# Kernel optimization log

Measured on AMD Instinct MI355X. Metric: run time of the kernel, lower is better.

Reference implementation:

```python
import jax, jax.numpy as jnp
import numpy as np

B, S, HID = 2, 2048, 2048
H, HKV, D = 8, 4, 256
SW = 1024
SOFTCAP = 50.0
SCALE = D ** -0.5
NEG = -2.3819763e38
ROPE_BASE = 10000.0


def _rope(x, cos, sin):
    # x: [B, S, H, D]; cos/sin: [S, D/2]. Gemma: first half real, second half imag.
    d2 = x.shape[-1] // 2
    x1, x2 = x[..., :d2], x[..., d2:]
    c = cos[None, :, None, :]
    s = sin[None, :, None, :]
    return jnp.concatenate([x1 * c - x2 * s, x1 * s + x2 * c], axis=-1)


def setup_inputs() -> dict:
    key = jax.random.key(0)
    k1, k2, k3, k4, k5, k6 = jax.random.split(key, 6)
    hidden_states = jax.random.normal(k1, (B, S, HID), dtype=jnp.float32)
    # Gemma RoPE freqs_cis -> cos/sin tables [S, D/2]
    inv_freq = 1.0 / (ROPE_BASE ** (np.arange(0, D, 2, dtype=np.float32) / D))
    t = np.arange(S, dtype=np.float32)
    ang = np.outer(t, inv_freq)  # [S, D/2]
    freqs_cos = jnp.asarray(np.cos(ang), dtype=jnp.float32)
    freqs_sin = jnp.asarray(np.sin(ang), dtype=jnp.float32)
    # causal additive mask [1,1,S,S]
    i = jnp.arange(S)
    causal = i[:, None] >= i[None, :]
    mask = jnp.where(causal, 0.0, NEG).astype(jnp.float32)[None, None]
    std = HID ** -0.5
    wq = jax.random.normal(k2, (H * D, HID), dtype=jnp.float32) * std
    wk = jax.random.normal(k3, (HKV * D, HID), dtype=jnp.float32) * std
    wv = jax.random.normal(k4, (HKV * D, HID), dtype=jnp.float32) * std
    wo = jax.random.normal(k5, (HID, H * D), dtype=jnp.float32) * (H * D) ** -0.5
    return {"hidden_states": hidden_states, "freqs_cos": freqs_cos,
            "freqs_sin": freqs_sin, "mask": mask,
            "wq": wq, "wk": wk, "wv": wv, "wo": wo}


def reference(hidden_states, freqs_cos, freqs_sin, mask, wq, wk, wv, wo):
    b, s, _ = hidden_states.shape
    q = (hidden_states @ wq.T).reshape(b, s, H, D)
    k = (hidden_states @ wk.T).reshape(b, s, HKV, D)
    v = (hidden_states @ wv.T).reshape(b, s, HKV, D)
    q = _rope(q, freqs_cos, freqs_sin)
    k = _rope(k, freqs_cos, freqs_sin)
    # GQA: repeat_interleave kv heads to match query heads
    rep = H // HKV
    k = jnp.repeat(k, rep, axis=2)
    v = jnp.repeat(v, rep, axis=2)
    q = q.transpose(0, 2, 1, 3)  # [B,H,S,D]
    k = k.transpose(0, 2, 1, 3)
    v = v.transpose(0, 2, 1, 3)
    # local (sliding window) mask: keep |i-j| <= SW-1, else NEG
    i = jnp.arange(s)
    rel = i[:, None] - i[None, :]
    sliding = jnp.abs(rel) < SW
    mask = jnp.where(sliding[None, None], mask, NEG)
    # scaled scores with tanh logit softcapping
    scores = jnp.einsum('bhqd,bhkd->bhqk', q * SCALE, k)
    scores = jnp.tanh(scores / SOFTCAP) * SOFTCAP
    scores = scores + mask
    probs = jax.nn.softmax(scores.astype(jnp.float32), axis=-1).astype(q.dtype)
    attn_output = jnp.einsum('bhqk,bhkd->bhqd', probs, v)  # [B,H,S,D]
    out = attn_output.transpose(0, 2, 1, 3).reshape(b, s, H * D) @ wo.T
    return out, probs, attn_output
```

## Files before the change

### kernel.cpp

```cpp
#include <hip/hip_runtime.h>
#include <hip/hip_bf16.h>

typedef __bf16 bfx8 __attribute__((ext_vector_type(8)));
typedef float  floatx4 __attribute__((ext_vector_type(4)));

#define B_   2
#define S_   2048
#define HID_ 2048
#define H_   8
#define HKV_ 4
#define D_   256
#define SW_  1024
#define NTOK (B_*S_)

__device__ __forceinline__ bool inputs_are_f32(const void* fc) {
  return *(const unsigned int*)fc == 0x3F800000u;
}

__device__ __forceinline__ bfx8 cvt8(const float* p) {
  floatx4 a = *(const floatx4*)p, b = *(const floatx4*)(p + 4);
  bfx8 r;
#pragma unroll
  for (int i = 0; i < 4; ++i) { r[i] = (__bf16)a[i]; r[i + 4] = (__bf16)b[i]; }
  return r;
}

__device__ __forceinline__ bfx8 ld8(const void* base, size_t eoff, bool f32m) {
  if (f32m) return cvt8((const float*)base + eoff);
  return *(const bfx8*)((const __bf16*)base + eoff);
}

__global__ __launch_bounds__(256)
void cvt_f32_bf16(const void* __restrict__ in, __bf16* __restrict__ out,
                  int n8, const void* __restrict__ fcp)
{
  const bool f32m = inputs_are_f32(fcp);
  int i = blockIdx.x * 256 + threadIdx.x;
  int stride = gridDim.x * 256;
  for (; i < n8; i += stride) {
    if (f32m) ((bfx8*)out)[i] = cvt8((const float*)in + (size_t)i * 8);
    else      ((bfx8*)out)[i] = ((const bfx8*)in)[i];
  }
}

template<int SWZ>
__device__ __forceinline__ void xcd_tile(int& bx, int& by) {
  int gx = gridDim.x;
  int orig = blockIdx.y * gx + blockIdx.x;
  int xcd = orig & 7, loc = orig >> 3;
  if (SWZ == 1) {
    int wpx = gx >> 3;
    if (wpx <= 1) { bx = xcd; by = loc; }
    else { bx = (xcd << 1) + (loc & 1); by = loc >> 1; }
  } else {
    int hpy = gridDim.y >> 3;
    int r = loc / gx;
    by = xcd * hpy + r;
    bx = loc - r * gx;
  }
}

template<int AMODE, int EPI, int DT, int SWZ>
__global__ __launch_bounds__(256)
void gemm_bt(const void* __restrict__ A, const void* __restrict__ Bm,
             void* __restrict__ C, const void* __restrict__ fcp,
             int K, int lda, int ldb, int ldc)
{
  const bool f32m = (DT == 1) ? false : inputs_are_f32(fcp);
  __shared__ __align__(16) __bf16 As[128*40];
  __shared__ __align__(16) __bf16 Bs[128*40];
  const int tid  = threadIdx.x;
  const int lane = tid & 63, wave = tid >> 6;
  int bx, by;
  xcd_tile<SWZ>(bx, by);
  const int m0 = by * 128, n0 = bx * 128;
  const int waveM = (wave >> 1) * 64, waveN = (wave & 1) * 64;
  const int lr = lane & 15, quad = lane >> 4;
  floatx4 acc[4][4] = {};

  for (int k0 = 0; k0 < K; k0 += 32) {
    __syncthreads();
#pragma unroll
    for (int cc = 0; cc < 2; ++cc) {
      int c = tid + cc * 256;
      int row = c >> 2, q = c & 3;
      bfx8 av;
      if (AMODE == 0) {
        av = ld8(A, (size_t)(m0 + row) * lda + (k0 + q * 8), f32m);
      } else {
        int mg = m0 + row, kk = k0 + q * 8;
        size_t aoff = ((size_t)((mg >> 11) * H_ + (kk >> 8)) * S_ + (mg & (S_ - 1))) * D_ + (kk & (D_ - 1));
        av = cvt8((const float*)A + aoff);
      }
      *(bfx8*)(&As[row * 40 + q * 8]) = av;
      *(bfx8*)(&Bs[row * 40 + q * 8]) = ld8(Bm, (size_t)(n0 + row) * ldb + (k0 + q * 8), f32m);
    }
    __syncthreads();
    bfx8 af[4], bfr[4];
#pragma unroll
    for (int im = 0; im < 4; ++im)
      af[im] = *(const bfx8*)(&As[(waveM + im * 16 + lr) * 40 + quad * 8]);
#pragma unroll
    for (int in = 0; in < 4; ++in)
      bfr[in] = *(const bfx8*)(&Bs[(waveN + in * 16 + lr) * 40 + quad * 8]);
#pragma unroll
    for (int im = 0; im < 4; ++im)
#pragma unroll
      for (int in = 0; in < 4; ++in)
        acc[im][in] = __builtin_amdgcn_mfma_f32_16x16x32_bf16(af[im], bfr[in], acc[im][in], 0, 0, 0);
  }

#pragma unroll
  for (int im = 0; im < 4; ++im)
#pragma unroll
    for (int in = 0; in < 4; ++in)
#pragma unroll
      for (int r = 0; r < 4; ++r) {
        int rg = m0 + waveM + im * 16 + quad * 4 + r;
        int cg = n0 + waveN + in * 16 + lr;
        float v = acc[im][in][r];
        if (EPI == 0) ((float*)C)[(size_t)rg * ldc + cg] = v;
        else          ((__bf16*)C)[(size_t)rg * ldc + cg] = (__bf16)v;
      }
}

__global__ __launch_bounds__(256)
void rope_kernel(float* __restrict__ qreg, float* __restrict__ kreg,
                 const void* __restrict__ fc, const void* __restrict__ fs)
{
  const bool f32m = inputs_are_f32(fc);
  int tok = blockIdx.x, t = threadIdx.x;
  int spos = tok & (S_ - 1);
  const float* qrow = qreg + (size_t)tok * 2048;
  const float* krow = kreg + (size_t)tok * 1024;
  float xq1[4], xq2[4], xk1[2], xk2[2];
#pragma unroll
  for (int p = 0; p < 4; ++p) {
    int idx = p * 256 + t, h = idx >> 7, d = idx & 127;
    xq1[p] = qrow[h * 256 + d]; xq2[p] = qrow[h * 256 + d + 128];
  }
#pragma unroll
  for (int p = 0; p < 2; ++p) {
    int idx = p * 256 + t, h = idx >> 7, d = idx & 127;
    xk1[p] = krow[h * 256 + d]; xk2[p] = krow[h * 256 + d + 128];
  }
  __syncthreads();
  __bf16* qo = (__bf16*)qreg + (size_t)tok * 4096;
  __bf16* ko = (__bf16*)kreg + (size_t)tok * 2048;
#pragma unroll
  for (int p = 0; p < 4; ++p) {
    int idx = p * 256 + t, h = idx >> 7, d = idx & 127;
    float c = f32m ? ((const float*)fc)[spos * 128 + d] : (float)((const __bf16*)fc)[spos * 128 + d];
    float s = f32m ? ((const float*)fs)[spos * 128 + d] : (float)((const __bf16*)fs)[spos * 128 + d];
    qo[h * 256 + d]       = (__bf16)((xq1[p] * c - xq2[p] * s) * 0.0625f);
    qo[h * 256 + d + 128] = (__bf16)((xq1[p] * s + xq2[p] * c) * 0.0625f);
  }
#pragma unroll
  for (int p = 0; p < 2; ++p) {
    int idx = p * 256 + t, h = idx >> 7, d = idx & 127;
    float c = f32m ? ((const float*)fc)[spos * 128 + d] : (float)((const __bf16*)fc)[spos * 128 + d];
    float s = f32m ? ((const float*)fs)[spos * 128 + d] : (float)((const __bf16*)fs)[spos * 128 + d];
    ko[h * 256 + d]       = (__bf16)(xk1[p] * c - xk2[p] * s);
    ko[h * 256 + d + 128] = (__bf16)(xk1[p] * s + xk2[p] * c);
  }
}

__global__ __launch_bounds__(256)
void qk_fused(const __bf16* __restrict__ qr, const __bf16* __restrict__ kr,
              float* __restrict__ probs)
{
  const int bh = blockIdx.y, b = bh >> 3, h = bh & 7, hkv = h >> 1;
  const int i0 = blockIdx.x * 64;
  __shared__ __align__(16) __bf16 Qs[64*256];
  __shared__ __align__(16) __bf16 Ks[64*256];
  const int tid = threadIdx.x, lane = tid & 63, wave = tid >> 6;
  const int lr = lane & 15, quad = lane >> 4;
  const int sx = lr & 7;
  const __bf16* qbase = qr + ((size_t)(b * S_ + i0) << 12) + h * D_;
  const __bf16* kbase = kr + ((size_t)(b * S_) << 11) + hkv * D_;

#pragma unroll
  for (int p = 0; p < 8; ++p) {
    int c = tid + p * 256;
    int row = c >> 5, ch = c & 31;
    *(bfx8*)(&Qs[row * 256 + (ch ^ (row & 7)) * 8]) =
        *(const bfx8*)(qbase + ((size_t)row << 12) + ch * 8);
  }

  const int jt0 = (i0 >= 1024) ? 0 : (16 - (i0 >> 6));
  const int myrow = wave * 16 + quad * 4;
  float psum[4] = {0.f, 0.f, 0.f, 0.f};
  float inv[4];

  for (int pass = 0; pass < 2; ++pass) {
    for (int jt = jt0; jt <= 16; ++jt) {
      int j0 = i0 - 1024 + jt * 64;
      __syncthreads();
#pragma unroll
      for (int p = 0; p < 8; ++p) {
        int c = tid + p * 256;
        int row = c >> 5, ch = c & 31;
        *(bfx8*)(&Ks[row * 256 + (ch ^ (row & 7)) * 8]) =
            *(const bfx8*)(kbase + ((size_t)(j0 + row) << 11) + ch * 8);
      }
      __syncthreads();
      floatx4 acc[4] = {};
#pragma unroll
      for (int ks = 0; ks < 8; ++ks) {
        bfx8 af = *(const bfx8*)(&Qs[(wave * 16 + lr) * 256 + ((ks * 4 + quad) ^ sx) * 8]);
#pragma unroll
        for (int in = 0; in < 4; ++in) {
          bfx8 bf = *(const bfx8*)(&Ks[(in * 16 + lr) * 256 + ((ks * 4 + quad) ^ sx) * 8]);
          acc[in] = __builtin_amdgcn_mfma_f32_16x16x32_bf16(af, bf, acc[in], 0, 0, 0);
        }
      }
#pragma unroll
      for (int in = 0; in < 4; ++in)
#pragma unroll
        for (int r = 0; r < 4; ++r) {
          int rg = i0 + myrow + r;
          int cg = j0 + in * 16 + lr;
          bool valid = (cg <= rg) && (rg - cg < SW_);
          float v = acc[in][r];
          float e = __expf(0.04f * v);
          float sc = 50.f * (e - 1.f) * __builtin_amdgcn_rcpf(e + 1.f);
          float pp = valid ? __expf(sc - 30.f) : 0.f;
          if (pass == 0) psum[r] += pp;
          else probs[((size_t)bh * S_ + rg) * 2048 + cg] = pp * inv[r];
        }
    }
    if (pass == 0) {
#pragma unroll
      for (int r = 0; r < 4; ++r) {
        float s = psum[r];
        s += __shfl_xor(s, 1); s += __shfl_xor(s, 2);
        s += __shfl_xor(s, 4); s += __shfl_xor(s, 8);
        inv[r] = 1.f / s;
      }
    }
  }

  {
    int L = (i0 >= 1024) ? (i0 - 1024) : 0;
    int R = i0 + 64;
    float* pb = probs + ((size_t)bh * S_ + i0) * 2048;
    int nL4 = L >> 2, nR4 = (2048 - R) >> 2;
    for (int r = 0; r < 64; ++r) {
      float* rowp = pb + (size_t)r * 2048;
      for (int c = tid; c < nL4; c += 256) ((floatx4*)rowp)[c] = (floatx4){0.f, 0.f, 0.f, 0.f};
      for (int c = tid; c < nR4; c += 256) *(floatx4*)(rowp + R + c * 4) = (floatx4){0.f, 0.f, 0.f, 0.f};
    }
  }
}

__global__ __launch_bounds__(256)
void transpose_v(const __bf16* __restrict__ vb, __bf16* __restrict__ vt)
{
  __shared__ __align__(16) __bf16 tile[64 * 72];
  int b = blockIdx.z, c0 = blockIdx.y * 64, j0 = blockIdx.x * 64;
  int tid = threadIdx.x;
#pragma unroll
  for (int p = 0; p < 2; ++p) {
    int e = p * 2048 + tid * 8;
    int row = e >> 6, col = e & 63;
    int swz = col ^ (((row >> 3) & 7) * 8);
    *(bfx8*)(&tile[row * 72 + swz]) =
      *(const bfx8*)(vb + ((size_t)(b * S_ + j0 + row) << 10) + c0 + col);
  }
  __syncthreads();
#pragma unroll
  for (int p = 0; p < 2; ++p) {
    int e = p * 2048 + tid * 8;
    int cc = e >> 6, jj = e & 63;
    bfx8 v8;
#pragma unroll
    for (int x = 0; x < 8; ++x) {
      int row = jj + x;
      v8[x] = tile[row * 72 + (cc ^ (((row >> 3) & 7) * 8))];
    }
    *(bfx8*)(vt + ((size_t)(b * 1024 + c0 + cc) << 11) + j0 + jj) = v8;
  }
}

__global__ __launch_bounds__(256)
void pv_wide(const float* __restrict__ probs, const __bf16* __restrict__ vt,
             float* __restrict__ attn)
{
  const int bh = blockIdx.y;
  const int b = bh >> 3, hkv = (bh & 7) >> 1;
  const int i0 = blockIdx.x * 128;
  const int kstart = (i0 >= 1024) ? (i0 - 1024) : 0;
  const int kend = i0 + 128;
  __shared__ __align__(16) __bf16 As[128*40];
  __shared__ __align__(16) __bf16 Bs[256*40];
  const int tid  = threadIdx.x;
  const int lane = tid & 63, wave = tid >> 6;
  const int waveM = (wave >> 1) * 64, waveN = (wave & 1) * 128;
  const int lr = lane & 15, quad = lane >> 4;
  floatx4 acc[4][8] = {};
  const float*  abase = probs + ((size_t)bh * S_) * 2048;
  const __bf16* bbase = vt + ((size_t)(b * 1024 + hkv * 256)) * 2048;

  for (int k0 = kstart; k0 < kend; k0 += 32) {
    __syncthreads();
#pragma unroll
    for (int p = 0; p < 6; ++p) {
      int c = tid + p * 256;
      if (p < 2) {
        int row = c >> 2, q = c & 3, kk = k0 + q * 8;
        *(bfx8*)(&As[row * 40 + q * 8]) = cvt8(abase + (size_t)(i0 + row) * 2048 + kk);
      } else {
        int c2 = c - 512;
        int row = c2 >> 2, q = c2 & 3, kk = k0 + q * 8;
        *(bfx8*)(&Bs[row * 40 + q * 8]) = *(const bfx8*)(bbase + ((size_t)row << 11) + kk);
      }
    }
    __syncthreads();
    bfx8 af[4];
#pragma unroll
    for (int im = 0; im < 4; ++im)
      af[im] = *(const bfx8*)(&As[(waveM + im * 16 + lr) * 40 + quad * 8]);
#pragma unroll
    for (int in = 0; in < 8; ++in) {
      bfx8 bf = *(const bfx8*)(&Bs[(waveN + in * 16 + lr) * 40 + quad * 8]);
#pragma unroll
      for (int im = 0; im < 4; ++im)
        acc[im][in] = __builtin_amdgcn_mfma_f32_16x16x32_bf16(af[im], bf, acc[im][in], 0, 0, 0);
    }
  }

#pragma unroll
  for (int im = 0; im < 4; ++im)
#pragma unroll
    for (int in = 0; in < 8; ++in)
#pragma unroll
      for (int r = 0; r < 4; ++r) {
        int rg = i0 + waveM + im * 16 + quad * 4 + r;
        int cg = waveN + in * 16 + lr;
        attn[((size_t)bh * S_ + rg) * D_ + cg] = acc[im][in][r];
      }
}

extern "C" void kernel_launch(void* const* d_in, const int* in_sizes, int n_in,
                              void* d_out, int out_size, void* d_ws, size_t ws_size,
                              hipStream_t stream) {
  (void)in_sizes; (void)n_in; (void)out_size; (void)d_ws; (void)ws_size;
  const void* hidden = d_in[0];
  const void* fc     = d_in[1];
  const void* fs     = d_in[2];
  const void* wq     = d_in[4];
  const void* wk     = d_in[5];
  const void* wv     = d_in[6];
  const void* wo     = d_in[7];

  float* out_r   = (float*)d_out;
  float* probs_r = out_r + (size_t)B_ * S_ * HID_;
  float* attn_r  = probs_r + (size_t)B_ * H_ * S_ * S_;

  float*  qf = attn_r;
  __bf16* qr = (__bf16*)attn_r;
  float*  kf = out_r;
  __bf16* kr = (__bf16*)out_r;
  __bf16* vb = (__bf16*)out_r + 8388608;
  __bf16* vt = (__bf16*)(out_r + 6291456);

  __bf16* hb  = (__bf16*)probs_r;
  __bf16* wqb = hb  + (size_t)NTOK * HID_;
  __bf16* wkb = wqb + (size_t)H_ * D_ * HID_;
  __bf16* wvb = wkb + (size_t)HKV_ * D_ * HID_;

  dim3 blk(256);
  cvt_f32_bf16<<<dim3(1024), blk, 0, stream>>>(hidden, hb,  NTOK * HID_ / 8, fc);
  cvt_f32_bf16<<<dim3(512),  blk, 0, stream>>>(wq, wqb, H_ * D_ * HID_ / 8, fc);
  cvt_f32_bf16<<<dim3(256),  blk, 0, stream>>>(wk, wkb, HKV_ * D_ * HID_ / 8, fc);
  cvt_f32_bf16<<<dim3(256),  blk, 0, stream>>>(wv, wvb, HKV_ * D_ * HID_ / 8, fc);

  gemm_bt<0,0,1,1><<<dim3(16,32), blk, 0, stream>>>(hb, wqb, qf, fc, 2048, 2048, 2048, 2048);
  gemm_bt<0,0,1,1><<<dim3(8,32),  blk, 0, stream>>>(hb, wkb, kf, fc, 2048, 2048, 2048, 1024);
  gemm_bt<0,1,1,1><<<dim3(8,32),  blk, 0, stream>>>(hb, wvb, vb, fc, 2048, 2048, 2048, 1024);
  rope_kernel<<<dim3(NTOK), blk, 0, stream>>>(qf, kf, fc, fs);
  transpose_v<<<dim3(32,16,2), blk, 0, stream>>>(vb, vt);
  qk_fused<<<dim3(32,16), blk, 0, stream>>>(qr, kr, probs_r);
  pv_wide<<<dim3(16,16), blk, 0, stream>>>(probs_r, vt, attn_r);
  gemm_bt<1,0,0,2><<<dim3(16,32), blk, 0, stream>>>(attn_r, wo, out_r, fc, 2048, 2048, 2048, 2048);
}
```

Baseline: 837.3 us.

## Fuse QKV projections into one GEMM and defer softmax normalization to PV

The three Q/K/V projection GEMMs become one launch over the concatenated weight matrix, which sits contiguously in memory. The epilogue routes each column region to the Q, K or V buffer, and the XCD tile swizzle is generalized to fit the wider grid. The QK kernel drops its second recompute pass: it writes unnormalized exponentials and stores per-row inverse sums in a scratch region. The PV kernel then scales each probability tile by that inverse sum, writes the normalized values back to the probs output, and uses them in the matmul. This removes half of the QK MFMA and transcendental work, at the cost of an extra read-modify-write of the probs band inside the PV kernel.

After: 800.6 us. 1.05x faster.

```diff
diff --git a/kernel.cpp b/kernel.cpp
--- a/kernel.cpp
+++ b/kernel.cpp
@@ -50,8 +50,8 @@
   int xcd = orig & 7, loc = orig >> 3;
   if (SWZ == 1) {
     int wpx = gx >> 3;
-    if (wpx <= 1) { bx = xcd; by = loc; }
-    else { bx = (xcd << 1) + (loc & 1); by = loc >> 1; }
+    bx = xcd * wpx + (loc & (wpx - 1));
+    by = loc / wpx;
   } else {
     int hpy = gridDim.y >> 3;
     int r = loc / gx;
@@ -125,6 +125,62 @@
 }
 
 __global__ __launch_bounds__(256)
+void gemm_qkv(const __bf16* __restrict__ A, const __bf16* __restrict__ Bm,
+              float* __restrict__ qf, float* __restrict__ kf,
+              __bf16* __restrict__ vb)
+{
+  __shared__ __align__(16) __bf16 As[128*40];
+  __shared__ __align__(16) __bf16 Bs[128*40];
+  const int tid  = threadIdx.x;
+  const int lane = tid & 63, wave = tid >> 6;
+  int bx, by;
+  xcd_tile<1>(bx, by);
+  const int m0 = by * 128, n0 = bx * 128;
+  const int region = n0 >> 10;
+  const int waveM = (wave >> 1) * 64, waveN = (wave & 1) * 64;
+  const int lr = lane & 15, quad = lane >> 4;
+  floatx4 acc[4][4] = {};
+
+  for (int k0 = 0; k0 < HID_; k0 += 32) {
+    __syncthreads();
+#pragma unroll
+    for (int cc = 0; cc < 2; ++cc) {
+      int c = tid + cc * 256;
+      int row = c >> 2, q = c & 3;
+      *(bfx8*)(&As[row * 40 + q * 8]) = *(const bfx8*)(A + (size_t)(m0 + row) * HID_ + (k0 + q * 8));
+      *(bfx8*)(&Bs[row * 40 + q * 8]) = *(const bfx8*)(Bm + (size_t)(n0 + row) * HID_ + (k0 + q * 8));
+    }
+    __syncthreads();
+    bfx8 af[4], bfr[4];
+#pragma unroll
+    for (int im = 0; im < 4; ++im)
+      af[im] = *(const bfx8*)(&As[(waveM + im * 16 + lr) * 40 + quad * 8]);
+#pragma unroll
+    for (int in = 0; in < 4; ++in)
+      bfr[in] = *(const bfx8*)(&Bs[(waveN + in * 16 + lr) * 40 + quad * 8]);
+#pragma unroll
+    for (int im = 0; im < 4; ++im)
+#pragma unroll
+      for (int in = 0; in < 4; ++in)
+        acc[im][in] = __builtin_amdgcn_mfma_f32_16x16x32_bf16(af[im], bfr[in], acc[im][in], 0, 0, 0);
+  }
+
+#pragma unroll
+  for (int im = 0; im < 4; ++im)
+#pragma unroll
+    for (int in = 0; in < 4; ++in)
+#pragma unroll
+      for (int r = 0; r < 4; ++r) {
+        int rg = m0 + waveM + im * 16 + quad * 4 + r;
+        int cg = n0 + waveN + in * 16 + lr;
+        float v = acc[im][in][r];
+        if (region < 2)       qf[(size_t)rg * 2048 + cg] = v;
+        else if (region == 2) kf[(size_t)rg * 1024 + (cg - 2048)] = v;
+        else                  vb[(size_t)rg * 1024 + (cg - 3072)] = (__bf16)v;
+      }
+}
+
+__global__ __launch_bounds__(256)
 void rope_kernel(float* __restrict__ qreg, float* __restrict__ kreg,
                  const void* __restrict__ fc, const void* __restrict__ fs)
 {
@@ -167,7 +223,7 @@
 
 __global__ __launch_bounds__(256)
 void qk_fused(const __bf16* __restrict__ qr, const __bf16* __restrict__ kr,
-              float* __restrict__ probs)
+              float* __restrict__ probs, float* __restrict__ sums_inv)
 {
   const int bh = blockIdx.y, b = bh >> 3, h = bh & 7, hkv = h >> 1;
   const int i0 = blockIdx.x * 64;
@@ -190,54 +246,50 @@
   const int jt0 = (i0 >= 1024) ? 0 : (16 - (i0 >> 6));
   const int myrow = wave * 16 + quad * 4;
   float psum[4] = {0.f, 0.f, 0.f, 0.f};
-  float inv[4];
-
-  for (int pass = 0; pass < 2; ++pass) {
-    for (int jt = jt0; jt <= 16; ++jt) {
-      int j0 = i0 - 1024 + jt * 64;
-      __syncthreads();
-#pragma unroll
-      for (int p = 0; p < 8; ++p) {
-        int c = tid + p * 256;
-        int row = c >> 5, ch = c & 31;
-        *(bfx8*)(&Ks[row * 256 + (ch ^ (row & 7)) * 8]) =
-            *(const bfx8*)(kbase + ((size_t)(j0 + row) << 11) + ch * 8);
-      }
-      __syncthreads();
-      floatx4 acc[4] = {};
-#pragma unroll
-      for (int ks = 0; ks < 8; ++ks) {
-        bfx8 af = *(const bfx8*)(&Qs[(wave * 16 + lr) * 256 + ((ks * 4 + quad) ^ sx) * 8]);
-#pragma unroll
-        for (int in = 0; in < 4; ++in) {
-          bfx8 bf = *(const bfx8*)(&Ks[(in * 16 + lr) * 256 + ((ks * 4 + quad) ^ sx) * 8]);
-          acc[in] = __builtin_amdgcn_mfma_f32_16x16x32_bf16(af, bf, acc[in], 0, 0, 0);
-        }
-      }
-#pragma unroll
-      for (int in = 0; in < 4; ++in)
-#pragma unroll
-        for (int r = 0; r < 4; ++r) {
-          int rg = i0 + myrow + r;
-          int cg = j0 + in * 16 + lr;
-          bool valid = (cg <= rg) && (rg - cg < SW_);
-          float v = acc[in][r];
-          float e = __expf(0.04f * v);
-          float sc = 50.f * (e - 1.f) * __builtin_amdgcn_rcpf(e + 1.f);
-          float pp = valid ? __expf(sc - 30.f) : 0.f;
-          if (pass == 0) psum[r] += pp;
-          else probs[((size_t)bh * S_ + rg) * 2048 + cg] = pp * inv[r];
-        }
-    }
-    if (pass == 0) {
+
+  for (int jt = jt0; jt <= 16; ++jt) {
+    int j0 = i0 - 1024 + jt * 64;
+    __syncthreads();
+#pragma unroll
+    for (int p = 0; p < 8; ++p) {
+      int c = tid + p * 256;
+      int row = c >> 5, ch = c & 31;
+      *(bfx8*)(&Ks[row * 256 + (ch ^ (row & 7)) * 8]) =
+          *(const bfx8*)(kbase + ((size_t)(j0 + row) << 11) + ch * 8);
+    }
+    __syncthreads();
+    floatx4 acc[4] = {};
+#pragma unroll
+    for (int ks = 0; ks < 8; ++ks) {
+      bfx8 af = *(const bfx8*)(&Qs[(wave * 16 + lr) * 256 + ((ks * 4 + quad) ^ sx) * 8]);
+#pragma unroll
+      for (int in = 0; in < 4; ++in) {
+        bfx8 bf = *(const bfx8*)(&Ks[(in * 16 + lr) * 256 + ((ks * 4 + quad) ^ sx) * 8]);
+        acc[in] = __builtin_amdgcn_mfma_f32_16x16x32_bf16(af, bf, acc[in], 0, 0, 0);
+      }
+    }
+#pragma unroll
+    for (int in = 0; in < 4; ++in)
 #pragma unroll
       for (int r = 0; r < 4; ++r) {
-        float s = psum[r];
-        s += __shfl_xor(s, 1); s += __shfl_xor(s, 2);
-        s += __shfl_xor(s, 4); s += __shfl_xor(s, 8);
-        inv[r] = 1.f / s;
-      }
-    }
+        int rg = i0 + myrow + r;
+        int cg = j0 + in * 16 + lr;
+        bool valid = (cg <= rg) && (rg - cg < SW_);
+        float v = acc[in][r];
+        float e = __expf(0.04f * v);
+        float sc = 50.f * (e - 1.f) * __builtin_amdgcn_rcpf(e + 1.f);
+        float pp = valid ? __expf(sc - 30.f) : 0.f;
+        psum[r] += pp;
+        probs[((size_t)bh * S_ + rg) * 2048 + cg] = pp;
+      }
+  }
+
+#pragma unroll
+  for (int r = 0; r < 4; ++r) {
+    float s = psum[r];
+    s += __shfl_xor(s, 1); s += __shfl_xor(s, 2);
+    s += __shfl_xor(s, 4); s += __shfl_xor(s, 8);
+    if (lr == 0) sums_inv[bh * 2048 + i0 + myrow + r] = 1.f / s;
   }
 
   {
@@ -283,8 +335,8 @@
 }
 
 __global__ __launch_bounds__(256)
-void pv_wide(const float* __restrict__ probs, const __bf16* __restrict__ vt,
-             float* __restrict__ attn)
+void pv_wide(float* __restrict__ probs, const __bf16* __restrict__ vt,
+             float* __restrict__ attn, const float* __restrict__ sums_inv)
 {
   const int bh = blockIdx.y;
   const int b = bh >> 3, hkv = (bh & 7) >> 1;
@@ -293,13 +345,16 @@
   const int kend = i0 + 128;
   __shared__ __align__(16) __bf16 As[128*40];
   __shared__ __align__(16) __bf16 Bs[256*40];
+  __shared__ float invs[128];
   const int tid  = threadIdx.x;
   const int lane = tid & 63, wave = tid >> 6;
   const int waveM = (wave >> 1) * 64, waveN = (wave & 1) * 128;
   const int lr = lane & 15, quad = lane >> 4;
   floatx4 acc[4][8] = {};
-  const float*  abase = probs + ((size_t)bh * S_) * 2048;
+  float*        abase = probs + ((size_t)bh * S_) * 2048;
   const __bf16* bbase = vt + ((size_t)(b * 1024 + hkv * 256)) * 2048;
+
+  if (tid < 128) invs[tid] = sums_inv[bh * 2048 + i0 + tid];
 
   for (int k0 = kstart; k0 < kend; k0 += 32) {
     __syncthreads();
@@ -308,7 +363,17 @@
       int c = tid + p * 256;
       if (p < 2) {
         int row = c >> 2, q = c & 3, kk = k0 + q * 8;
-        *(bfx8*)(&As[row * 40 + q * 8]) = cvt8(abase + (size_t)(i0 + row) * 2048 + kk);
+        float iv = invs[row];
+        float* ap = abase + (size_t)(i0 + row) * 2048 + kk;
+        floatx4 a0 = *(const floatx4*)ap, a1 = *(const floatx4*)(ap + 4);
+        bfx8 rb;
+#pragma unroll
+        for (int e = 0; e < 4; ++e) {
+          a0[e] *= iv; a1[e] *= iv;
+          rb[e] = (__bf16)a0[e]; rb[e + 4] = (__bf16)a1[e];
+        }
+        *(floatx4*)ap = a0; *(floatx4*)(ap + 4) = a1;
+        *(bfx8*)(&As[row * 40 + q * 8]) = rb;
       } else {
         int c2 = c - 512;
         int row = c2 >> 2, q = c2 & 3, kk = k0 + q * 8;
@@ -363,6 +428,7 @@
   __bf16* kr = (__bf16*)out_r;
   __bf16* vb = (__bf16*)out_r + 8388608;
   __bf16* vt = (__bf16*)(out_r + 6291456);
+  float* sums_inv = out_r + 4194304;
 
   __bf16* hb  = (__bf16*)probs_r;
   __bf16* wqb = hb  + (size_t)NTOK * HID_;
@@ -375,12 +441,10 @@
   cvt_f32_bf16<<<dim3(256),  blk, 0, stream>>>(wk, wkb, HKV_ * D_ * HID_ / 8, fc);
   cvt_f32_bf16<<<dim3(256),  blk, 0, stream>>>(wv, wvb, HKV_ * D_ * HID_ / 8, fc);
 
-  gemm_bt<0,0,1,1><<<dim3(16,32), blk, 0, stream>>>(hb, wqb, qf, fc, 2048, 2048, 2048, 2048);
-  gemm_bt<0,0,1,1><<<dim3(8,32),  blk, 0, stream>>>(hb, wkb, kf, fc, 2048, 2048, 2048, 1024);
-  gemm_bt<0,1,1,1><<<dim3(8,32),  blk, 0, stream>>>(hb, wvb, vb, fc, 2048, 2048, 2048, 1024);
+  gemm_qkv<<<dim3(32,32), blk, 0, stream>>>(hb, wqb, qf, kf, vb);
   rope_kernel<<<dim3(NTOK), blk, 0, stream>>>(qf, kf, fc, fs);
   transpose_v<<<dim3(32,16,2), blk, 0, stream>>>(vb, vt);
-  qk_fused<<<dim3(32,16), blk, 0, stream>>>(qr, kr, probs_r);
-  pv_wide<<<dim3(16,16), blk, 0, stream>>>(probs_r, vt, attn_r);
+  qk_fused<<<dim3(32,16), blk, 0, stream>>>(qr, kr, probs_r, sums_inv);
+  pv_wide<<<dim3(16,16), blk, 0, stream>>>(probs_r, vt, attn_r, sums_inv);
   gemm_bt<1,0,0,2><<<dim3(16,32), blk, 0, stream>>>(attn_r, wo, out_r, fc, 2048, 2048, 2048, 2048);
 }
```
